# Optimization experiments

Hardware: AMD Instinct MI355X
Metric: run time of the kernel (lower is better)

## Reference

```python
import jax, jax.numpy as jnp
import numpy as np

B, T = 64, 256
IN, HID, OUT = 512, 1024, 256
NUM_DOMAINS = 20

def setup_inputs() -> dict:
    key = jax.random.key(0)
    k1, k2, k3, k4 = jax.random.split(key, 4)
    x = jax.random.normal(k1, (B, T, IN), dtype=jnp.float32)
    hetero_info = jax.random.randint(k2, (B, 2), 0, NUM_DOMAINS, dtype=jnp.int64)
    # embedding tables init N(0, 0.02) as in the torch module
    fc1_table = 0.02 * jax.random.normal(k3, (NUM_DOMAINS, IN * HID + HID), dtype=jnp.float32)
    fc2_table = 0.02 * jax.random.normal(k4, (NUM_DOMAINS, HID * OUT + OUT), dtype=jnp.float32)
    return {"x": x, "hetero_info": hetero_info, "fc1_table": fc1_table, "fc2_table": fc2_table}

def reference(x, hetero_info, fc1_table, fc2_table):
    domain_id = hetero_info[:, 0].astype(jnp.int32)
    Bn = domain_id.shape[0]
    fc1_param = fc1_table[domain_id]                     # (B, IN*HID + HID)
    w1 = fc1_param[:, : IN * HID].reshape(Bn, IN, HID)   # (B, IN, HID)
    b1 = fc1_param[:, IN * HID:].reshape(Bn, 1, HID)
    fc2_param = fc2_table[domain_id]                     # (B, HID*OUT + OUT)
    w2 = fc2_param[:, : HID * OUT].reshape(Bn, HID, OUT) # (B, HID, OUT)
    b2 = fc2_param[:, HID * OUT:].reshape(Bn, 1, OUT)
    h = jnp.einsum('bti,bih->bth', x, w1) + b1
    h = jax.nn.gelu(h, approximate=False)  # torch nn.GELU default = exact erf
    out = jnp.einsum('bth,bho->bto', h, w2) + b2
    return out
```

## Files before the change

kernel.cpp:

```cpp
#include <hip/hip_runtime.h>
#include <math.h>

#define B_  64
#define T_  256
#define IN_ 512
#define HID_ 1024
#define OUT_ 256
#define NDOM 20

typedef __bf16 bf16_t;
typedef __bf16 bf16x8 __attribute__((ext_vector_type(8)));
typedef float  f32x4  __attribute__((ext_vector_type(4)));

__device__ __forceinline__ unsigned f2bf_bits(float f) {
    unsigned u = __builtin_bit_cast(unsigned, f);
    return (u + 0x7FFFu + ((u >> 16) & 1u)) >> 16;
}
__device__ __forceinline__ unsigned pack_bf16x2(float x, float y) {
    return f2bf_bits(x) | (f2bf_bits(y) << 16);
}

__device__ __forceinline__ void gl_lds16(const void* g, void* l) {
    __builtin_amdgcn_global_load_lds(
        (const __attribute__((address_space(1))) unsigned*)g,
        (__attribute__((address_space(3))) unsigned*)l,
        16, 0, 0);
}

__global__ __launch_bounds__(256) void cvt_x(
    const float* __restrict__ X, bf16_t* __restrict__ Xbf)
{
    const size_t idx = (size_t)blockIdx.x * 256 + threadIdx.x;
    float4 v = ((const float4*)X)[idx];
    uint2 p;
    p.x = pack_bf16x2(v.x, v.y);
    p.y = pack_bf16x2(v.z, v.w);
    ((uint2*)Xbf)[idx] = p;
}

template<int K, int N>
__global__ __launch_bounds__(256) void cvt_transpose(
    const float* __restrict__ table, bf16_t* __restrict__ Wt, float* __restrict__ BiasOut)
{
    const int d  = blockIdx.z;
    const float* W = table + (size_t)d * ((size_t)K * N + N);
    const int n0 = blockIdx.x * 64;
    const int k0 = blockIdx.y * 64;
    const int tid = threadIdx.x;

    __shared__ float t[64][65];

    #pragma unroll
    for (int r = 0; r < 4; ++r) {
        const int kl = (tid >> 4) + r * 16;
        const int nl = (tid & 15) * 4;
        float4 v = *(const float4*)(W + (size_t)(k0 + kl) * N + n0 + nl);
        t[kl][nl + 0] = v.x; t[kl][nl + 1] = v.y;
        t[kl][nl + 2] = v.z; t[kl][nl + 3] = v.w;
    }
    __syncthreads();

    bf16_t* Wtd = Wt + (size_t)d * K * N;
    #pragma unroll
    for (int r = 0; r < 4; ++r) {
        const int nl = (tid >> 4) + r * 16;
        const int k4 = (tid & 15) * 4;
        uint2 p;
        p.x = pack_bf16x2(t[k4 + 0][nl], t[k4 + 1][nl]);
        p.y = pack_bf16x2(t[k4 + 2][nl], t[k4 + 3][nl]);
        *(uint2*)(Wtd + (size_t)(n0 + nl) * K + k0 + k4) = p;
    }

    if (blockIdx.y == 0 && tid < 64)
        BiasOut[(size_t)d * N + n0 + tid] = W[(size_t)K * N + n0 + tid];
}

#define CT_STRIDE 136
__global__ __launch_bounds__(256) void fc1_gemm(
    const bf16_t* __restrict__ Xbf,
    const bf16_t* __restrict__ W1t,
    const float*  __restrict__ Bias,
    const int*    __restrict__ hetero,
    bf16_t*       __restrict__ H)
{
    const int id   = blockIdx.x;
    const int g    = id & 127;
    const int nidx = id >> 7;
    const int b    = g >> 1;
    const int m0   = (g & 1) * 128;
    const int n0   = nidx * 128;
    const int d    = hetero[2 * b];
    const bf16_t* W    = W1t + (size_t)d * HID_ * IN_;
    const float*  bias = Bias + (size_t)d * HID_;
    const bf16_t* A    = Xbf + (size_t)(b * 256 + m0) * IN_;

    __shared__ __attribute__((aligned(16))) char smem[128 * CT_STRIDE * 2];
    bf16_t* LdsA = (bf16_t*)smem;
    bf16_t* LdsB = (bf16_t*)(smem + 16384);
    bf16_t* Ct   = (bf16_t*)smem;

    const int tid  = threadIdx.x;
    const int wave = tid >> 6;
    const int lane = tid & 63;
    const int l16  = lane & 15;
    const int quad = lane >> 4;
    const int wm   = (wave >> 1) * 64;
    const int wn   = (wave & 1) * 64;

    f32x4 acc[4][4] = {};

    for (int kk = 0; kk < IN_; kk += 64) {
        #pragma unroll
        for (int cc = 0; cc < 4; ++cc) {
            const int r0  = wave * 32 + cc * 8;
            const int row = r0 + (lane >> 3);
            const int cs  = (lane & 7) ^ (row & 7);
            gl_lds16(A + (size_t)row * IN_ + kk + cs * 8, &LdsA[r0 * 64]);
        }
        #pragma unroll
        for (int cc = 0; cc < 4; ++cc) {
            const int r0  = wave * 32 + cc * 8;
            const int row = r0 + (lane >> 3);
            const int cs  = (lane & 7) ^ (row & 7);
            gl_lds16(W + (size_t)(n0 + row) * IN_ + kk + cs * 8, &LdsB[r0 * 64]);
        }
        __syncthreads();

        #pragma unroll
        for (int h = 0; h < 2; ++h) {
            bf16x8 af[4], bfg[4];
            #pragma unroll
            for (int i = 0; i < 4; ++i) {
                const int r = wm + i * 16 + l16;
                const int c = (h * 4 + quad) ^ (r & 7);
                af[i] = *(const bf16x8*)&LdsA[r * 64 + c * 8];
            }
            #pragma unroll
            for (int j = 0; j < 4; ++j) {
                const int r = wn + j * 16 + l16;
                const int c = (h * 4 + quad) ^ (r & 7);
                bfg[j] = *(const bf16x8*)&LdsB[r * 64 + c * 8];
            }
            #pragma unroll
            for (int i = 0; i < 4; ++i)
                #pragma unroll
                for (int j = 0; j < 4; ++j)
                    acc[i][j] = __builtin_amdgcn_mfma_f32_16x16x32_bf16(bfg[j], af[i], acc[i][j], 0, 0, 0);
        }
        __syncthreads();
    }

    #pragma unroll
    for (int i = 0; i < 4; ++i) {
        const int m = wm + i * 16 + l16;
        #pragma unroll
        for (int j = 0; j < 4; ++j) {
            const int nl = wn + j * 16 + quad * 4;
            const float4 b4 = *(const float4*)&bias[n0 + nl];
            float v0 = acc[i][j][0] + b4.x;
            float v1 = acc[i][j][1] + b4.y;
            float v2 = acc[i][j][2] + b4.z;
            float v3 = acc[i][j][3] + b4.w;
            v0 = 0.5f * v0 * (1.0f + erff(v0 * 0.70710678f));
            v1 = 0.5f * v1 * (1.0f + erff(v1 * 0.70710678f));
            v2 = 0.5f * v2 * (1.0f + erff(v2 * 0.70710678f));
            v3 = 0.5f * v3 * (1.0f + erff(v3 * 0.70710678f));
            uint2 p;
            p.x = pack_bf16x2(v0, v1);
            p.y = pack_bf16x2(v2, v3);
            *(uint2*)&Ct[m * CT_STRIDE + nl] = p;
        }
    }
    __syncthreads();

    #pragma unroll
    for (int it = 0; it < 8; ++it) {
        const int row = it * 16 + (tid >> 4);
        const int ch  = tid & 15;
        uint4 v = *(const uint4*)&Ct[row * CT_STRIDE + ch * 8];
        *(uint4*)&H[((size_t)(b * 256 + m0 + row)) * HID_ + n0 + ch * 8] = v;
    }
}

__global__ __launch_bounds__(256) void fc2_gemm(
    const bf16_t* __restrict__ H,
    const bf16_t* __restrict__ W2t,
    const float*  __restrict__ Bias,
    const int*    __restrict__ hetero,
    float*        __restrict__ Out)
{
    const int id   = blockIdx.x;
    const int g    = id & 255;
    const int nidx = id >> 8;
    const int b    = g >> 2;
    const int m0   = (g & 3) * 64;
    const int n0   = nidx * 64;
    const int d    = hetero[2 * b];
    const bf16_t* W    = W2t + (size_t)d * OUT_ * HID_;
    const float*  bias = Bias + (size_t)d * OUT_;

    __shared__ __attribute__((aligned(16))) bf16_t LdsA[64 * 64];
    __shared__ __attribute__((aligned(16))) bf16_t LdsB[64 * 64];

    const int tid  = threadIdx.x;
    const int wave = tid >> 6;
    const int lane = tid & 63;
    const int l16  = lane & 15;
    const int quad = lane >> 4;
    const int wm   = (wave >> 1) * 32;
    const int wn   = (wave & 1) * 32;

    f32x4 acc[2][2] = {};

    for (int kk = 0; kk < HID_; kk += 64) {
        #pragma unroll
        for (int cc = 0; cc < 2; ++cc) {
            const int r0  = wave * 16 + cc * 8;
            const int row = r0 + (lane >> 3);
            const int cs  = (lane & 7) ^ (row & 7);
            gl_lds16(H + (size_t)(b * 256 + m0 + row) * HID_ + kk + cs * 8,
                     &LdsA[r0 * 64]);
        }
        #pragma unroll
        for (int cc = 0; cc < 2; ++cc) {
            const int r0  = wave * 16 + cc * 8;
            const int row = r0 + (lane >> 3);
            const int cs  = (lane & 7) ^ (row & 7);
            gl_lds16(W + (size_t)(n0 + row) * HID_ + kk + cs * 8,
                     &LdsB[r0 * 64]);
        }
        __syncthreads();

        #pragma unroll
        for (int h = 0; h < 2; ++h) {
            bf16x8 af[2], bfg[2];
            #pragma unroll
            for (int i = 0; i < 2; ++i) {
                const int r = wm + i * 16 + l16;
                const int c = (h * 4 + quad) ^ (r & 7);
                af[i] = *(const bf16x8*)&LdsA[r * 64 + c * 8];
            }
            #pragma unroll
            for (int j = 0; j < 2; ++j) {
                const int r = wn + j * 16 + l16;
                const int c = (h * 4 + quad) ^ (r & 7);
                bfg[j] = *(const bf16x8*)&LdsB[r * 64 + c * 8];
            }
            #pragma unroll
            for (int i = 0; i < 2; ++i)
                #pragma unroll
                for (int j = 0; j < 2; ++j)
                    acc[i][j] = __builtin_amdgcn_mfma_f32_16x16x32_bf16(bfg[j], af[i], acc[i][j], 0, 0, 0);
        }
        __syncthreads();
    }

    #pragma unroll
    for (int i = 0; i < 2; ++i) {
        const int m = m0 + wm + i * 16 + l16;
        #pragma unroll
        for (int j = 0; j < 2; ++j) {
            const int nl = wn + j * 16 + quad * 4;
            const float4 b4 = *(const float4*)&bias[n0 + nl];
            float4 o;
            o.x = acc[i][j][0] + b4.x;
            o.y = acc[i][j][1] + b4.y;
            o.z = acc[i][j][2] + b4.z;
            o.w = acc[i][j][3] + b4.w;
            *(float4*)&Out[(size_t)(b * 256 + m) * OUT_ + n0 + nl] = o;
        }
    }
}

extern "C" void kernel_launch(void* const* d_in, const int* in_sizes, int n_in,
                              void* d_out, int out_size, void* d_ws, size_t ws_size,
                              hipStream_t stream) {
    const float* x         = (const float*)d_in[0];
    const int*   hetero    = (const int*)d_in[1];
    const float* fc1_table = (const float*)d_in[2];
    const float* fc2_table = (const float*)d_in[3];
    float*       out       = (float*)d_out;

    char* ws = (char*)d_ws;
    bf16_t* W1t = (bf16_t*)(ws);
    bf16_t* W2t = (bf16_t*)(ws + 20971520);
    float*  b1  = (float*)(ws + 31457280);
    float*  b2  = (float*)(ws + 31539200);
    bf16_t* H   = (bf16_t*)(ws + 31559680);

    bf16_t* Xbf = (bf16_t*)d_out;

    cvt_x<<<dim3(8192), 256, 0, stream>>>(x, Xbf);
    cvt_transpose<IN_, HID_><<<dim3(HID_ / 64, IN_ / 64, NDOM), 256, 0, stream>>>(
        fc1_table, W1t, b1);
    cvt_transpose<HID_, OUT_><<<dim3(OUT_ / 64, HID_ / 64, NDOM), 256, 0, stream>>>(
        fc2_table, W2t, b2);

    fc1_gemm<<<dim3(1024), 256, 0, stream>>>(Xbf, W1t, b1, hetero, H);
    fc2_gemm<<<dim3(1024), 256, 0, stream>>>(H, W2t, b2, hetero, out);
}
```

Before: 188.6 us.

## Merge conversion kernels into one prepass and double fc2 K-tile

```diff
diff --git a/kernel.cpp b/kernel.cpp
--- a/kernel.cpp
+++ b/kernel.cpp
@@ -27,28 +27,45 @@
         16, 0, 0);
 }
 
-__global__ __launch_bounds__(256) void cvt_x(
-    const float* __restrict__ X, bf16_t* __restrict__ Xbf)
+__global__ __launch_bounds__(256) void prepass(
+    const float* __restrict__ X,  bf16_t* __restrict__ Xbf,
+    const float* __restrict__ t1, bf16_t* __restrict__ W1t, float* __restrict__ b1,
+    const float* __restrict__ t2, bf16_t* __restrict__ W2t, float* __restrict__ b2)
 {
-    const size_t idx = (size_t)blockIdx.x * 256 + threadIdx.x;
-    float4 v = ((const float4*)X)[idx];
-    uint2 p;
-    p.x = pack_bf16x2(v.x, v.y);
-    p.y = pack_bf16x2(v.z, v.w);
-    ((uint2*)Xbf)[idx] = p;
-}
-
-template<int K, int N>
-__global__ __launch_bounds__(256) void cvt_transpose(
-    const float* __restrict__ table, bf16_t* __restrict__ Wt, float* __restrict__ BiasOut)
-{
-    const int d  = blockIdx.z;
+    const int bid = blockIdx.x;
+    const int tid = threadIdx.x;
+
+    if (bid < 8192) {
+        const size_t idx = (size_t)bid * 256 + tid;
+        float4 v = ((const float4*)X)[idx];
+        uint2 p;
+        p.x = pack_bf16x2(v.x, v.y);
+        p.y = pack_bf16x2(v.z, v.w);
+        ((uint2*)Xbf)[idx] = p;
+        return;
+    }
+
+    __shared__ float t[64][65];
+
+    const float* table; bf16_t* Wt; float* Bias;
+    int K, N, d, n0, k0;
+    if (bid < 10752) {
+        const int r = bid - 8192;
+        K = IN_; N = HID_;
+        d = r >> 7;
+        n0 = (r & 15) * 64;
+        k0 = ((r >> 4) & 7) * 64;
+        table = t1; Wt = W1t; Bias = b1;
+    } else {
+        const int r = bid - 10752;
+        K = HID_; N = OUT_;
+        d = r >> 6;
+        n0 = (r & 3) * 64;
+        k0 = ((r >> 2) & 15) * 64;
+        table = t2; Wt = W2t; Bias = b2;
+    }
+
     const float* W = table + (size_t)d * ((size_t)K * N + N);
-    const int n0 = blockIdx.x * 64;
-    const int k0 = blockIdx.y * 64;
-    const int tid = threadIdx.x;
-
-    __shared__ float t[64][65];
 
     #pragma unroll
     for (int r = 0; r < 4; ++r) {
@@ -71,8 +88,8 @@
         *(uint2*)(Wtd + (size_t)(n0 + nl) * K + k0 + k4) = p;
     }
 
-    if (blockIdx.y == 0 && tid < 64)
-        BiasOut[(size_t)d * N + n0 + tid] = W[(size_t)K * N + n0 + tid];
+    if (k0 == 0 && tid < 64)
+        Bias[(size_t)d * N + n0 + tid] = W[(size_t)K * N + n0 + tid];
 }
 
 #define CT_STRIDE 136
@@ -199,8 +216,8 @@
     const bf16_t* W    = W2t + (size_t)d * OUT_ * HID_;
     const float*  bias = Bias + (size_t)d * OUT_;
 
-    __shared__ __attribute__((aligned(16))) bf16_t LdsA[64 * 64];
-    __shared__ __attribute__((aligned(16))) bf16_t LdsB[64 * 64];
+    __shared__ __attribute__((aligned(16))) bf16_t LdsA[64 * 128];
+    __shared__ __attribute__((aligned(16))) bf16_t LdsB[64 * 128];
 
     const int tid  = threadIdx.x;
     const int wave = tid >> 6;
@@ -212,39 +229,39 @@
 
     f32x4 acc[2][2] = {};
 
-    for (int kk = 0; kk < HID_; kk += 64) {
-        #pragma unroll
-        for (int cc = 0; cc < 2; ++cc) {
-            const int r0  = wave * 16 + cc * 8;
-            const int row = r0 + (lane >> 3);
-            const int cs  = (lane & 7) ^ (row & 7);
+    for (int kk = 0; kk < HID_; kk += 128) {
+        #pragma unroll
+        for (int cc = 0; cc < 4; ++cc) {
+            const int r0  = wave * 16 + cc * 4;
+            const int row = r0 + (lane >> 4);
+            const int cs  = (lane & 15) ^ (row & 15);
             gl_lds16(H + (size_t)(b * 256 + m0 + row) * HID_ + kk + cs * 8,
-                     &LdsA[r0 * 64]);
-        }
-        #pragma unroll
-        for (int cc = 0; cc < 2; ++cc) {
-            const int r0  = wave * 16 + cc * 8;
-            const int row = r0 + (lane >> 3);
-            const int cs  = (lane & 7) ^ (row & 7);
+                     &LdsA[r0 * 128]);
+        }
+        #pragma unroll
+        for (int cc = 0; cc < 4; ++cc) {
+            const int r0  = wave * 16 + cc * 4;
+            const int row = r0 + (lane >> 4);
+            const int cs  = (lane & 15) ^ (row & 15);
             gl_lds16(W + (size_t)(n0 + row) * HID_ + kk + cs * 8,
-                     &LdsB[r0 * 64]);
+                     &LdsB[r0 * 128]);
         }
         __syncthreads();
 
         #pragma unroll
-        for (int h = 0; h < 2; ++h) {
+        for (int h = 0; h < 4; ++h) {
             bf16x8 af[2], bfg[2];
             #pragma unroll
             for (int i = 0; i < 2; ++i) {
                 const int r = wm + i * 16 + l16;
-                const int c = (h * 4 + quad) ^ (r & 7);
-                af[i] = *(const bf16x8*)&LdsA[r * 64 + c * 8];
+                const int c = (h * 4 + quad) ^ (r & 15);
+                af[i] = *(const bf16x8*)&LdsA[r * 128 + c * 8];
             }
             #pragma unroll
             for (int j = 0; j < 2; ++j) {
                 const int r = wn + j * 16 + l16;
-                const int c = (h * 4 + quad) ^ (r & 7);
-                bfg[j] = *(const bf16x8*)&LdsB[r * 64 + c * 8];
+                const int c = (h * 4 + quad) ^ (r & 15);
+                bfg[j] = *(const bf16x8*)&LdsB[r * 128 + c * 8];
             }
             #pragma unroll
             for (int i = 0; i < 2; ++i)
@@ -290,11 +307,8 @@
 
     bf16_t* Xbf = (bf16_t*)d_out;
 
-    cvt_x<<<dim3(8192), 256, 0, stream>>>(x, Xbf);
-    cvt_transpose<IN_, HID_><<<dim3(HID_ / 64, IN_ / 64, NDOM), 256, 0, stream>>>(
-        fc1_table, W1t, b1);
-    cvt_transpose<HID_, OUT_><<<dim3(OUT_ / 64, HID_ / 64, NDOM), 256, 0, stream>>>(
-        fc2_table, W2t, b2);
+    prepass<<<dim3(12032), 256, 0, stream>>>(
+        x, Xbf, fc1_table, W1t, b1, fc2_table, W2t, b2);
 
     fc1_gemm<<<dim3(1024), 256, 0, stream>>>(Xbf, W1t, b1, hetero, H);
     fc2_gemm<<<dim3(1024), 256, 0, stream>>>(H, W2t, b2, hetero, out);
```

New measurement: 189.5 us. About the same (+0.5%).
